# Kernel optimization log

Hardware: AMD Instinct MI355X
Metric: run time of the kernel (lower is better)

Reference implementation:

```python
import jax, jax.numpy as jnp
import numpy as np


def setup_inputs() -> dict:
    key = jax.random.key(0)
    k1, k2, k3 = jax.random.split(key, 3)
    L, B, D = 2048, 32, 512  # seq_len, batch, input_size == hidden_size == output_size
    NUM_MATRICES = 3  # has_skip_term and input_size == output_size
    x = jax.random.normal(k1, (L, B, D), dtype=jnp.float32)
    # transform_module: Linear(D, D * 3, bias=False), xavier_uniform-like scale
    W = jax.random.normal(k2, (D, D * NUM_MATRICES), dtype=jnp.float32) * (1.0 / np.sqrt(D))
    # weight_c ~ U(-weight_c_init, weight_c_init), shape (2*D,)
    weight_c = jax.random.uniform(k3, (2 * D,), dtype=jnp.float32, minval=-1.0, maxval=1.0)
    # bias: zeros; highway_bias (=0.0) added to second half -> all zeros
    bias = jnp.zeros((2 * D,), dtype=jnp.float32)
    return {"x": x, "W": W, "weight_c": weight_c, "bias": bias}


def reference(x, W, weight_c, bias):
    # x: (L, B, D); W: (D, 3D); weight_c, bias: (2D,)
    L, B, D = x.shape
    # U = transform_module(x): batched matmul, then view as (L, B, D, 3)
    U = jnp.einsum('lbi,io->lbo', x, W).reshape(L, B, D, 3)
    wc_f, wc_r = weight_c[:D], weight_c[D:]  # forget / reset peephole weights
    b_f, b_r = bias[:D], bias[D:]            # forget / reset (highway) biases

    def step(c_prev, inp):
        u, res = inp  # u: (B, D, 3); res: (B, D) residual (= x_t, skip term)
        fg = jax.nn.sigmoid(u[..., 1] + wc_f * c_prev + b_f)
        rg = jax.nn.sigmoid(u[..., 2] + wc_r * c_prev + b_r)
        c = fg * c_prev + (1.0 - fg) * u[..., 0]
        # activation_type == 0 -> g(c) = c; scale_val is None (rescale=False)
        h = rg * c + (1.0 - rg) * res
        return c, h

    c0 = jnp.zeros((B, D), dtype=x.dtype)
    c_last, h = jax.lax.scan(step, c0, (U, x))
    return h, c_last
```

## Files before the change

kernel.cpp:

```cpp
#include <hip/hip_runtime.h>

#define LL 2048
#define BB 32
#define DD 512
#define MM (LL * BB)
#define NN (3 * DD)
#define KK (DD)

typedef short bf16x8 __attribute__((ext_vector_type(8)));
typedef float f32x4 __attribute__((ext_vector_type(4)));

__device__ __forceinline__ unsigned short f2bf(float f) {
  unsigned u = __builtin_bit_cast(unsigned, f);
  u += 0x7fffu + ((u >> 16) & 1u);
  return (unsigned short)(u >> 16);
}
__device__ __forceinline__ float bf2f(unsigned short h) {
  unsigned u = (unsigned)h << 16;
  return __builtin_bit_cast(float, u);
}
__device__ __forceinline__ void lds_cp16(unsigned short* lds, const unsigned short* g) {
  __builtin_amdgcn_global_load_lds(
      (const __attribute__((address_space(1))) void*)g,
      (__attribute__((address_space(3))) void*)lds, 16, 0, 0);
}

__global__ __launch_bounds__(256) void cvt_x_kernel(const float* __restrict__ x,
                                                    unsigned short* __restrict__ xb) {
  int i = blockIdx.x * 256 + threadIdx.x;
  float4 v = ((const float4*)x)[i];
  ushort4 o;
  o.x = f2bf(v.x); o.y = f2bf(v.y); o.z = f2bf(v.z); o.w = f2bf(v.w);
  ((ushort4*)xb)[i] = o;
}

__global__ __launch_bounds__(256) void cvt_w_kernel(const float* __restrict__ W,
                                                    unsigned short* __restrict__ Wt) {
  int j = blockIdx.x * 256 + threadIdx.x;
  int i  = j & (KK - 1);
  int op = j >> 9;
  int g  = op >> 9;
  int dd = op & (DD - 1);
  Wt[j] = f2bf(W[(size_t)i * NN + dd * 3 + g]);
}

__global__ __launch_bounds__(256) void gemm_kernel(const unsigned short* __restrict__ A,
                                                   const unsigned short* __restrict__ Bt,
                                                   unsigned short* __restrict__ U) {
  __shared__ __align__(16) unsigned short sA[128 * 32];
  __shared__ __align__(16) unsigned short sB[128 * 32];
  const int tn = blockIdx.x * 128;
  const int tm = blockIdx.y * 128;
  const int lane = threadIdx.x & 63;
  const int wv   = threadIdx.x >> 6;
  const int wm = (wv & 1) * 64;
  const int wn = (wv >> 1) * 64;
  const int quad = lane >> 4;
  const int l16  = lane & 15;

  f32x4 acc[4][4] = {};

  const int srow = lane >> 2;
  const int scol = (lane & 3) * 8;

  for (int k0 = 0; k0 < KK; k0 += 32) {
#pragma unroll
    for (int t = 0; t < 2; ++t) {
      int seg = wv * 2 + t;
      int row = seg * 16 + srow;
      lds_cp16(&sA[seg * 512], &A [(size_t)(tm + row) * KK + k0 + scol]);
      lds_cp16(&sB[seg * 512], &Bt[(size_t)(tn + row) * KK + k0 + scol]);
    }
    __syncthreads();

    bf16x8 af[4], bf[4];
#pragma unroll
    for (int i = 0; i < 4; ++i) {
      af[i] = *(const bf16x8*)&sA[(wm + i * 16 + l16) * 32 + quad * 8];
      bf[i] = *(const bf16x8*)&sB[(wn + i * 16 + l16) * 32 + quad * 8];
    }
#pragma unroll
    for (int i = 0; i < 4; ++i)
#pragma unroll
      for (int j = 0; j < 4; ++j)
        acc[i][j] = __builtin_amdgcn_mfma_f32_16x16x32_bf16(af[i], bf[j], acc[i][j], 0, 0, 0);
    __syncthreads();
  }

#pragma unroll
  for (int i = 0; i < 4; ++i)
#pragma unroll
    for (int j = 0; j < 4; ++j)
#pragma unroll
      for (int r = 0; r < 4; ++r) {
        int row = tm + wm + i * 16 + quad * 4 + r;
        int col = tn + wn + j * 16 + l16;
        U[(size_t)row * NN + col] = f2bf(acc[i][j][r]);
      }
}

#define SCH 32
#define NCH (LL / SCH)

__global__ __launch_bounds__(128, 1) void scan_kernel(const unsigned short* __restrict__ U,
                                                      const unsigned short* __restrict__ xb,
                                                      const float* __restrict__ wc,
                                                      const float* __restrict__ bias,
                                                      float* __restrict__ out) {
  __shared__ __align__(16) unsigned short lds[2][SCH * 256];

  const int wv   = threadIdx.x >> 6;
  const int lane = threadIdx.x & 63;
  const int b  = blockIdx.x >> 3;
  const int d0 = (blockIdx.x & 7) << 6;

  if (wv == 1) {
    const int half = lane >> 5;
    const int r    = lane & 31;
    const int st   = r >> 3;
    const int idx  = r & 7;
    const unsigned short* gp;
    size_t stride;
    if (st < 3) { gp = U  + (size_t)b * NN + st * DD + d0 + idx * 8; stride = (size_t)BB * NN; }
    else        { gp = xb + (size_t)b * DD + d0 + idx * 8;           stride = (size_t)BB * DD; }
    gp += (size_t)half * stride;
    const size_t adv = stride * 2;

#pragma unroll
    for (int s = 0; s < SCH / 2; ++s) { lds_cp16(&lds[0][s * 512], gp); gp += adv; }
    __syncthreads();
    for (int i = 0; i < NCH; ++i) {
      if (i + 1 < NCH) {
        unsigned short* lb = &lds[(i + 1) & 1][0];
#pragma unroll
        for (int s = 0; s < SCH / 2; ++s) { lds_cp16(&lb[s * 512], gp); gp += adv; }
      }
      __syncthreads();
    }
  } else {
    const int d = d0 + lane;
    const float kln = 1.442695040888963f;
    const float wcf = wc[d],      wcr = wc[DD + d];
    const float pf0 = -kln * bias[d],       pr0 = -kln * bias[DD + d];
    const float pf1 = -kln * wcf,           pr1 = -kln * wcr;
    float* hp = out + (size_t)b * DD + d;
    float c = 0.0f;

    __syncthreads();
    for (int i = 0; i < NCH; ++i) {
      const unsigned short* lb = &lds[i & 1][0];
#pragma unroll
      for (int s = 0; s < SCH; ++s) {
        float u0 = bf2f(lb[s * 256 +       lane]);
        float u1 = bf2f(lb[s * 256 +  64 + lane]);
        float u2 = bf2f(lb[s * 256 + 128 + lane]);
        float xr = bf2f(lb[s * 256 + 192 + lane]);
        float tf = __builtin_fmaf(pf1, c, __builtin_fmaf(-kln, u1, pf0));
        float tr = __builtin_fmaf(pr1, c, __builtin_fmaf(-kln, u2, pr0));
        float fg = __builtin_amdgcn_rcpf(1.0f + __builtin_amdgcn_exp2f(tf));
        float rg = __builtin_amdgcn_rcpf(1.0f + __builtin_amdgcn_exp2f(tr));
        c = __builtin_fmaf(fg, c - u0, u0);
        *hp = __builtin_fmaf(rg, c - xr, xr);
        hp += BB * DD;
      }
      __syncthreads();
    }
    out[(size_t)LL * BB * DD + (size_t)b * DD + d] = c;
  }
}

extern "C" void kernel_launch(void* const* d_in, const int* in_sizes, int n_in,
                              void* d_out, int out_size, void* d_ws, size_t ws_size,
                              hipStream_t stream) {
  const float* x    = (const float*)d_in[0];
  const float* W    = (const float*)d_in[1];
  const float* wc   = (const float*)d_in[2];
  const float* bias = (const float*)d_in[3];
  float* out = (float*)d_out;

  unsigned short* xb = (unsigned short*)d_ws;
  unsigned short* Wt = xb + (size_t)MM * KK;
  unsigned short* U  = Wt + (size_t)NN * KK;

  cvt_x_kernel<<<(MM * KK) / (4 * 256), 256, 0, stream>>>(x, xb);
  cvt_w_kernel<<<(NN * KK) / 256, 256, 0, stream>>>(W, Wt);
  gemm_kernel<<<dim3(NN / 128, MM / 128), 256, 0, stream>>>(xb, Wt, U);
  scan_kernel<<<(BB * DD) / 64, 128, 0, stream>>>(U, xb, wc, bias, out);
}
```

Measured before the change: 471.2 us.

## Reorder x and U layouts batch-major with vectorized stores, LDS swizzle, XCD tile mapping

The bf16 copy of x is now stored batch-major ([B][L][D]), so the GEMM's M rows are ordered by batch then time. The GEMM writes U as packed 4-row groups with 8-byte vector stores instead of scalar 2-byte stores. It also XOR-swizzles LDS rows to avoid bank conflicts and remaps 1D block ids so each XCD gets contiguous M tiles. The scan producer wave is rewritten to fetch contiguous per-batch time chunks, and the consumer reads four timesteps of U per vector LDS load. This trades more complex indexing for coalesced global traffic in both the GEMM epilogue and the scan loads.

```diff
diff --git a/kernel.cpp b/kernel.cpp
--- a/kernel.cpp
+++ b/kernel.cpp
@@ -28,10 +28,14 @@
 __global__ __launch_bounds__(256) void cvt_x_kernel(const float* __restrict__ x,
                                                     unsigned short* __restrict__ xb) {
   int i = blockIdx.x * 256 + threadIdx.x;
+  int l   = i >> 12;
+  int rem = i & 4095;
+  int b   = rem >> 7;
+  int dg  = rem & 127;
   float4 v = ((const float4*)x)[i];
   ushort4 o;
   o.x = f2bf(v.x); o.y = f2bf(v.y); o.z = f2bf(v.z); o.w = f2bf(v.w);
-  ((ushort4*)xb)[i] = o;
+  ((ushort4*)xb)[((size_t)b * LL + l) * 128 + dg] = o;
 }
 
 __global__ __launch_bounds__(256) void cvt_w_kernel(const float* __restrict__ W,
@@ -49,8 +53,12 @@
                                                    unsigned short* __restrict__ U) {
   __shared__ __align__(16) unsigned short sA[128 * 32];
   __shared__ __align__(16) unsigned short sB[128 * 32];
-  const int tn = blockIdx.x * 128;
-  const int tm = blockIdx.y * 128;
+  const int n   = blockIdx.x;
+  const int xcd = n & 7;
+  const int i2  = n >> 3;
+  const int mt  = xcd * 64 + i2 / 12;
+  const int nt  = i2 % 12;
+  const int tm = mt * 128, tn = nt * 128;
   const int lane = threadIdx.x & 63;
   const int wv   = threadIdx.x >> 6;
   const int wm = (wv & 1) * 64;
@@ -61,7 +69,9 @@
   f32x4 acc[4][4] = {};
 
   const int srow = lane >> 2;
-  const int scol = (lane & 3) * 8;
+  const int scol = (((lane & 3) ^ ((lane >> 3) & 3))) * 8;
+  const int aoff = (wm + l16) * 32 + ((quad ^ ((l16 >> 1) & 3)) * 8);
+  const int boff = (wn + l16) * 32 + ((quad ^ ((l16 >> 1) & 3)) * 8);
 
   for (int k0 = 0; k0 < KK; k0 += 32) {
 #pragma unroll
@@ -76,8 +86,8 @@
     bf16x8 af[4], bf[4];
 #pragma unroll
     for (int i = 0; i < 4; ++i) {
-      af[i] = *(const bf16x8*)&sA[(wm + i * 16 + l16) * 32 + quad * 8];
-      bf[i] = *(const bf16x8*)&sB[(wn + i * 16 + l16) * 32 + quad * 8];
+      af[i] = *(const bf16x8*)&sA[aoff + i * 512];
+      bf[i] = *(const bf16x8*)&sB[boff + i * 512];
     }
 #pragma unroll
     for (int i = 0; i < 4; ++i)
@@ -88,15 +98,17 @@
   }
 
 #pragma unroll
-  for (int i = 0; i < 4; ++i)
-#pragma unroll
-    for (int j = 0; j < 4; ++j)
-#pragma unroll
-      for (int r = 0; r < 4; ++r) {
-        int row = tm + wm + i * 16 + quad * 4 + r;
-        int col = tn + wn + j * 16 + l16;
-        U[(size_t)row * NN + col] = f2bf(acc[i][j][r]);
-      }
+  for (int i = 0; i < 4; ++i) {
+    size_t rb = (size_t)((tm + wm + i * 16) >> 2) + quad;
+#pragma unroll
+    for (int j = 0; j < 4; ++j) {
+      int col = tn + wn + j * 16 + l16;
+      ushort4 o;
+      o.x = f2bf(acc[i][j][0]); o.y = f2bf(acc[i][j][1]);
+      o.z = f2bf(acc[i][j][2]); o.w = f2bf(acc[i][j][3]);
+      *(ushort4*)&U[(rb * NN + col) * 4] = o;
+    }
+  }
 }
 
 #define SCH 32
@@ -115,28 +127,38 @@
   const int d0 = (blockIdx.x & 7) << 6;
 
   if (wv == 1) {
-    const int half = lane >> 5;
-    const int r    = lane & 31;
-    const int st   = r >> 3;
-    const int idx  = r & 7;
-    const unsigned short* gp;
-    size_t stride;
-    if (st < 3) { gp = U  + (size_t)b * NN + st * DD + d0 + idx * 8; stride = (size_t)BB * NN; }
-    else        { gp = xb + (size_t)b * DD + d0 + idx * 8;           stride = (size_t)BB * DD; }
-    gp += (size_t)half * stride;
-    const size_t adv = stride * 2;
-
-#pragma unroll
-    for (int s = 0; s < SCH / 2; ++s) { lds_cp16(&lds[0][s * 512], gp); gp += adv; }
+    const int h   = lane >> 5;
+    const int c16 = lane & 31;
+    const int xs  = lane >> 3;
+    const int xc  = lane & 7;
+
+#define LOAD_CHUNK(ch, buf)                                                  \
+    do {                                                                     \
+      unsigned short* lb_ = &lds[buf][0];                                    \
+      _Pragma("unroll") for (int w = 0; w < 12; ++w) {                       \
+        int q  = 2 * w + h;                        \
+        int g  = q >> 3;                                                     \
+        int lb2 = q & 7;                                                     \
+        const unsigned short* gp =                                           \
+            U + ((size_t)(b * 512 + (ch) * 8 + lb2) * NN + g * DD + d0) * 4  \
+              + c16 * 8;                                                     \
+        lds_cp16(lb_ + w * 512, gp);                                         \
+      }                                                                      \
+      _Pragma("unroll") for (int v = 0; v < 4; ++v) {                        \
+        int s = v * 8 + xs;                                                  \
+        const unsigned short* gp =                                           \
+            xb + ((size_t)(b * LL + (ch) * 32 + s)) * DD + d0 + xc * 8;      \
+        lds_cp16(lb_ + 6144 + v * 512, gp);                                  \
+      }                                                                      \
+    } while (0)
+
+    LOAD_CHUNK(0, 0);
     __syncthreads();
     for (int i = 0; i < NCH; ++i) {
-      if (i + 1 < NCH) {
-        unsigned short* lb = &lds[(i + 1) & 1][0];
-#pragma unroll
-        for (int s = 0; s < SCH / 2; ++s) { lds_cp16(&lb[s * 512], gp); gp += adv; }
-      }
+      if (i + 1 < NCH) LOAD_CHUNK(i + 1, (i + 1) & 1);
       __syncthreads();
     }
+#undef LOAD_CHUNK
   } else {
     const int d = d0 + lane;
     const float kln = 1.442695040888963f;
@@ -148,20 +170,30 @@
 
     __syncthreads();
     for (int i = 0; i < NCH; ++i) {
-      const unsigned short* lb = &lds[i & 1][0];
-#pragma unroll
-      for (int s = 0; s < SCH; ++s) {
-        float u0 = bf2f(lb[s * 256 +       lane]);
-        float u1 = bf2f(lb[s * 256 +  64 + lane]);
-        float u2 = bf2f(lb[s * 256 + 128 + lane]);
-        float xr = bf2f(lb[s * 256 + 192 + lane]);
-        float tf = __builtin_fmaf(pf1, c, __builtin_fmaf(-kln, u1, pf0));
-        float tr = __builtin_fmaf(pr1, c, __builtin_fmaf(-kln, u2, pr0));
-        float fg = __builtin_amdgcn_rcpf(1.0f + __builtin_amdgcn_exp2f(tf));
-        float rg = __builtin_amdgcn_rcpf(1.0f + __builtin_amdgcn_exp2f(tr));
-        c = __builtin_fmaf(fg, c - u0, u0);
-        *hp = __builtin_fmaf(rg, c - xr, xr);
-        hp += BB * DD;
+      const unsigned short* lb_ = &lds[i & 1][0];
+#pragma unroll
+      for (int blk = 0; blk < 8; ++blk) {
+        ushort4 U0 = *(const ushort4*)&lb_[       blk * 256 + lane * 4];
+        ushort4 U1 = *(const ushort4*)&lb_[2048 + blk * 256 + lane * 4];
+        ushort4 U2 = *(const ushort4*)&lb_[4096 + blk * 256 + lane * 4];
+        const unsigned short* u0p = (const unsigned short*)&U0;
+        const unsigned short* u1p = (const unsigned short*)&U1;
+        const unsigned short* u2p = (const unsigned short*)&U2;
+#pragma unroll
+        for (int r = 0; r < 4; ++r) {
+          int s = blk * 4 + r;
+          float u0 = bf2f(u0p[r]);
+          float u1 = bf2f(u1p[r]);
+          float u2 = bf2f(u2p[r]);
+          float xr = bf2f(lb_[6144 + s * 64 + lane]);
+          float tf = __builtin_fmaf(pf1, c, __builtin_fmaf(-kln, u1, pf0));
+          float tr = __builtin_fmaf(pr1, c, __builtin_fmaf(-kln, u2, pr0));
+          float fg = __builtin_amdgcn_rcpf(1.0f + __builtin_amdgcn_exp2f(tf));
+          float rg = __builtin_amdgcn_rcpf(1.0f + __builtin_amdgcn_exp2f(tr));
+          c = __builtin_fmaf(fg, c - u0, u0);
+          *hp = __builtin_fmaf(rg, c - xr, xr);
+          hp += BB * DD;
+        }
       }
       __syncthreads();
     }
@@ -184,6 +216,6 @@
 
   cvt_x_kernel<<<(MM * KK) / (4 * 256), 256, 0, stream>>>(x, xb);
   cvt_w_kernel<<<(NN * KK) / 256, 256, 0, stream>>>(W, Wt);
-  gemm_kernel<<<dim3(NN / 128, MM / 128), 256, 0, stream>>>(xb, Wt, U);
+  gemm_kernel<<<(MM / 128) * (NN / 128), 256, 0, stream>>>(xb, Wt, U);
   scan_kernel<<<(BB * DD) / 64, 128, 0, stream>>>(U, xb, wc, bias, out);
 }
```

New measurement: 458.7 us. 1.03x faster.
